# Kernel tuning notes

Measured on AMD Instinct MI355X. Metric: run time of the kernel, lower is better.

## Reference

```python
import jax, jax.numpy as jnp
import numpy as np
import math

E = 16          # num_experts
K = 2           # top_k
CAP_FACTOR = 1.25
TEMP = 1.0      # router_temperature


def setup_inputs() -> dict:
    key = jax.random.key(0)
    ks = jax.random.split(key, 4)
    B, F, H, O = 16384, 1024, 4096, 1024
    features = jax.random.normal(ks[0], (B, F), dtype=jnp.float32)
    Wg = jax.random.normal(ks[1], (E, F), dtype=jnp.float32) / np.sqrt(F)
    bg = jnp.zeros((E,), jnp.float32)
    W1 = jax.random.normal(ks[2], (E, F, H), dtype=jnp.float32) / np.sqrt(F)
    b1 = jnp.zeros((E, H), jnp.float32)
    W2 = jax.random.normal(ks[3], (E, H, O), dtype=jnp.float32) / np.sqrt(H)
    b2 = jnp.zeros((E, O), jnp.float32)
    expert_bias = jnp.zeros((E,), jnp.float32)
    return {"features": features, "Wg": Wg, "bg": bg, "W1": W1, "b1": b1,
            "W2": W2, "b2": b2, "expert_bias": expert_bias}


def reference(features, Wg, bg, W1, b1, W2, b2, expert_bias):
    B, F = features.shape
    O = W2.shape[-1]
    cap = max(1, int(math.ceil(CAP_FACTOR * B * K / E)))  # per-expert capacity

    # --- router: scores = W_g * features + expert_bias (no noise) ---
    scores = features @ Wg.T + bg + expert_bias[None, :]            # [B,E]
    topk_scores, topk_idx = jax.lax.top_k(scores, K)                # [B,K]
    topk_w = jax.nn.softmax(topk_scores / TEMP, axis=1)             # [B,K]

    # per-(token,expert) assignment and mixing weight
    onehot = topk_idx[:, :, None] == jnp.arange(E)[None, None, :]   # [B,K,E]
    assign = jnp.any(onehot, axis=1)                                # [B,E]
    w = jnp.sum(topk_w[:, :, None] * onehot.astype(topk_w.dtype), axis=1)  # [B,E]

    # capacity: first `cap` tokens (ascending index, matching torch.nonzero order)
    pos = jnp.cumsum(assign.astype(jnp.int32), axis=0) - 1          # [B,E]
    keep = assign & (pos < cap)
    pos_safe = jnp.where(keep, pos, cap)                            # dropped -> overflow slot

    # inverse map: inv[e,c] = token index filling slot c of expert e (B if empty)
    e_grid = jnp.broadcast_to(jnp.arange(E)[None, :], (B, E))
    b_grid = jnp.broadcast_to(jnp.arange(B, dtype=jnp.int32)[:, None], (B, E))
    inv = jnp.full((E, cap + 1), B, dtype=jnp.int32)
    inv = inv.at[e_grid, pos_safe].set(b_grid)[:, :cap]             # [E,cap]

    # dispatch (gather) into per-expert buffers
    feats_pad = jnp.concatenate([features, jnp.zeros((1, F), features.dtype)], axis=0)
    buf = feats_pad[inv]                                            # [E,cap,F]

    # experts: Linear -> ReLU -> Linear, batched over experts
    h = jax.nn.relu(jnp.einsum('ecf,efh->ech', buf, W1) + b1[:, None, :])
    y = jnp.einsum('ech,eho->eco', h, W2) + b2[:, None, :]          # [E,cap,O]

    # weighted combine (scatter-add back to tokens; empty slots have weight 0)
    w_pad = jnp.concatenate([w, jnp.zeros((1, E), w.dtype)], axis=0)  # [B+1,E]
    w_slot = w_pad[inv, jnp.arange(E)[:, None]]                     # [E,cap]
    out = jnp.zeros((B + 1, O), features.dtype)
    out = out.at[inv.reshape(-1)].add((w_slot[..., None] * y).reshape(-1, O))
    return out[:B]
```

## Files before the change

kernel.cpp:

```cpp
#include <hip/hip_runtime.h>
#include <math.h>


typedef __attribute__((ext_vector_type(8))) short bf16x8;
typedef __attribute__((ext_vector_type(4))) float floatx4;

static __device__ __forceinline__ unsigned short f2bf(float f) {
  union { float f; unsigned u; } v; v.f = f;
  unsigned u = v.u;
  return (unsigned short)((u + 0x7fffu + ((u >> 16) & 1u)) >> 16);
}

static __device__ __forceinline__ void gload_lds16(const void* g, void* l) {
  __builtin_amdgcn_global_load_lds(
      (const __attribute__((address_space(1))) unsigned int*)g,
      (__attribute__((address_space(3))) unsigned int*)l, 16, 0, 0);
}

__global__ void k_cvt_bf16(const float* __restrict__ src,
                           unsigned short* __restrict__ dst, long n4) {
  long i = (long)blockIdx.x * blockDim.x + threadIdx.x;
  if (i >= n4) return;
  float4 f = ((const float4*)src)[i];
  ushort4 o;
  o.x = f2bf(f.x); o.y = f2bf(f.y); o.z = f2bf(f.z); o.w = f2bf(f.w);
  ((ushort4*)dst)[i] = o;
}

__global__ void k_txp_bf16(const float* __restrict__ src,
                           unsigned short* __restrict__ dst, int Kd, int Nd) {
  __shared__ float tile[32][33];
  int e = blockIdx.z;
  int n0 = blockIdx.x * 32;
  int k0 = blockIdx.y * 32;
  int tx = threadIdx.x;
  int ty = threadIdx.y;
  const float* s = src + (size_t)e * Kd * Nd;
#pragma unroll
  for (int j = 0; j < 4; ++j) {
    int k = ty + j * 8;
    tile[k][tx] = s[(size_t)(k0 + k) * Nd + n0 + tx];
  }
  __syncthreads();
  unsigned short* d = dst + (size_t)e * Kd * Nd;
#pragma unroll
  for (int j = 0; j < 4; ++j) {
    int n = ty + j * 8;
    d[(size_t)(n0 + n) * Kd + k0 + tx] = f2bf(tile[tx][n]);
  }
}

__global__ __launch_bounds__(256) void k_gating(
    const float* __restrict__ feat, const float* __restrict__ Wg,
    const float* __restrict__ bg, const float* __restrict__ ebias,
    int* __restrict__ topki, float* __restrict__ topkw,
    int* __restrict__ hist, int B, int F) {
  __shared__ float WgS[16 * 1024];
  for (int i = threadIdx.x; i < 16 * F; i += blockDim.x) WgS[i] = Wg[i];
  __syncthreads();
  int lane = threadIdx.x & 63;
  int wid = threadIdx.x >> 6;
  int gw = blockIdx.x * 4 + wid;
  int nw = gridDim.x * 4;
  int per = B / nw;
  for (int it = 0; it < per; ++it) {
    int t = gw * per + it;
    double acc[16];
#pragma unroll
    for (int e = 0; e < 16; ++e) acc[e] = 0.0;
    const float* fr = feat + (size_t)t * F;
    for (int c = 0; c < F / 64; ++c) {
      double fd = (double)fr[c * 64 + lane];
#pragma unroll
      for (int e = 0; e < 16; ++e)
        acc[e] += fd * (double)WgS[e * F + c * 64 + lane];
    }
#pragma unroll
    for (int e = 0; e < 16; ++e) {
#pragma unroll
      for (int off = 32; off >= 1; off >>= 1)
        acc[e] += __shfl_xor(acc[e], off);
    }
    double s[16];
#pragma unroll
    for (int e = 0; e < 16; ++e)
      s[e] = acc[e] + (double)bg[e] + (double)ebias[e];
    int e1 = 0; double s1 = s[0];
#pragma unroll
    for (int e = 1; e < 16; ++e) if (s[e] > s1) { s1 = s[e]; e1 = e; }
    int e2 = -1; double s2 = -1e300;
#pragma unroll
    for (int e = 0; e < 16; ++e)
      if (e != e1 && s[e] > s2) { s2 = s[e]; e2 = e; }
    double d = exp(s2 - s1);
    float w1 = (float)(1.0 / (1.0 + d));
    float w2 = (float)(d / (1.0 + d));
    if (lane == 0) {
      topki[t * 2 + 0] = e1; topki[t * 2 + 1] = e2;
      topkw[t * 2 + 0] = w1; topkw[t * 2 + 1] = w2;
      atomicAdd(&hist[(t >> 8) * 16 + e1], 1);
      atomicAdd(&hist[(t >> 8) * 16 + e2], 1);
    }
  }
}

__global__ void k_scan(const int* __restrict__ hist, int* __restrict__ choff,
                       int* __restrict__ cntcl, int nchunk, int cap) {
  int e = threadIdx.x;
  if (e < 16) {
    int off = 0;
    for (int c = 0; c < nchunk; ++c) {
      choff[c * 16 + e] = off;
      off += hist[c * 16 + e];
    }
    cntcl[e] = off < cap ? off : cap;
  }
}

__global__ __launch_bounds__(64) void k_build(
    const int* __restrict__ topki, const float* __restrict__ topkw,
    const int* __restrict__ choff, int* __restrict__ list,
    float* __restrict__ wlist, int cap, int capR) {
  int c = blockIdx.x;
  int lane = threadIdx.x;
  int run[16];
#pragma unroll
  for (int e = 0; e < 16; ++e) run[e] = choff[c * 16 + e];
  unsigned long long below = (lane == 63) ? 0x7fffffffffffffffull
                                          : ((1ull << lane) - 1ull);
  for (int r = 0; r < 4; ++r) {
    int t = c * 256 + r * 64 + lane;
    int e1 = topki[t * 2 + 0], e2 = topki[t * 2 + 1];
    float w1 = topkw[t * 2 + 0], w2 = topkw[t * 2 + 1];
    int p1 = -1, p2 = -1;
#pragma unroll
    for (int e = 0; e < 16; ++e) {
      unsigned long long m = __ballot(e1 == e) | __ballot(e2 == e);
      int rk = run[e] + __popcll(m & below);
      if (e1 == e) p1 = rk;
      if (e2 == e) p2 = rk;
      run[e] += __popcll(m);
    }
    if (p1 >= 0 && p1 < cap) { list[e1 * capR + p1] = t; wlist[e1 * capR + p1] = w1; }
    if (p2 >= 0 && p2 < cap) { list[e2 * capR + p2] = t; wlist[e2 * capR + p2] = w2; }
  }
}

__global__ void k_padfill(const int* __restrict__ cntcl, int* __restrict__ list,
                          float* __restrict__ wlist, int capR) {
  int e = blockIdx.x;
  int cnt = cntcl[e];
  for (int s = cnt + (int)threadIdx.x; s < capR; s += (int)blockDim.x) {
    list[e * capR + s] = 0;
    wlist[e * capR + s] = 0.0f;
  }
}

#define VM_WAIT4 asm volatile("s_waitcnt vmcnt(4)" ::: "memory")
#define VM_WAIT0 asm volatile("s_waitcnt vmcnt(0)" ::: "memory")

template <int MODE>
__global__ __launch_bounds__(512, 2) void k_gemm(
    const unsigned short* __restrict__ A, const unsigned short* __restrict__ Bt,
    const float* __restrict__ bias, const int* __restrict__ list,
    const float* __restrict__ wlist, const int* __restrict__ cntcl,
    unsigned short* __restrict__ Hout, float* __restrict__ out,
    int Kd, int Nd, int RT, int NT, int capR) {
  __shared__ __align__(16) char smem[98304];

  int nwg = gridDim.x;
  int qq = nwg >> 3, rr = nwg & 7;
  int xcd = blockIdx.x & 7, idx = blockIdx.x >> 3;
  int bid = (xcd < rr ? xcd * (qq + 1) : rr * (qq + 1) + (xcd - rr) * qq) + idx;

  int e = bid / (RT * NT);
  int rt = (bid / NT) % RT;
  int nt = bid % NT;
  int cnt = cntcl[e];
  int r0 = rt * 256;
  if (r0 >= cnt) return;
  int n0 = nt * 256;

  int tid = threadIdx.x;
  int lane = tid & 63;
  int wid = tid >> 6;
  int wr = wid >> 2;
  int wc = wid & 3;
  int l16 = lane & 15, q = lane >> 4;

  int srow = wid * 16 + (lane >> 2);
  int cg = (lane & 3) ^ ((lane >> 3) & 3);
  const char* pA[2];
  const char* pB[2];
#pragma unroll
  for (int rnd = 0; rnd < 2; ++rnd) {
    int r = rnd * 128 + srow;
    const unsigned short* arow;
    if (MODE == 0) {
      int tok = list[e * capR + r0 + r];
      arow = A + (size_t)tok * Kd;
    } else {
      arow = A + (size_t)(e * capR + r0 + r) * Kd;
    }
    pA[rnd] = (const char*)arow + cg * 16;
    pB[rnd] = (const char*)(Bt + (size_t)e * Nd * Kd + (size_t)(n0 + r) * Kd) +
              cg * 16;
  }
  unsigned stbase = wid * 1024;

#define STAGE(tt, bufi)                                   \
  do {                                                    \
    char* dst_ = smem + (bufi) * 32768 + stbase;          \
    int off_ = (tt) * 64;                                 \
    gload_lds16(pA[0] + off_, dst_);                      \
    gload_lds16(pA[1] + off_, dst_ + 8192);               \
    gload_lds16(pB[0] + off_, dst_ + 16384);              \
    gload_lds16(pB[1] + off_, dst_ + 16384 + 8192);       \
  } while (0)

  floatx4 acc[8][4];
#pragma unroll
  for (int i = 0; i < 8; ++i)
#pragma unroll
    for (int j = 0; j < 4; ++j) acc[i][j] = 0.0f;

  int sw = ((q ^ ((lane >> 1) & 3)) << 4);
  int arl = wr * 128 + l16;
  int brl = wc * 64 + l16;

  int nk = Kd / 32;

  STAGE(0, 0);
  STAGE(1, 1);
  VM_WAIT4;
  __builtin_amdgcn_s_barrier();

  int cur = 0;
  for (int t = 0; t < nk; ++t) {
    const char* Ab = smem + cur * 32768;
    const char* Bb = Ab + 16384;
    bool pre = (t + 2) < nk;
    int nx2 = cur + 2; if (nx2 >= 3) nx2 -= 3;

    bf16x8 af[4], bfr[4];
#pragma unroll
    for (int i = 0; i < 4; ++i)
      af[i] = *(const bf16x8*)(Ab + (arl + i * 16) * 64 + sw);
#pragma unroll
    for (int j = 0; j < 4; ++j)
      bfr[j] = *(const bf16x8*)(Bb + (brl + j * 16) * 64 + sw);
    if (pre) STAGE(t + 2, nx2);
    __builtin_amdgcn_s_barrier();
    __builtin_amdgcn_s_setprio(1);
#pragma unroll
    for (int i = 0; i < 4; ++i)
#pragma unroll
      for (int j = 0; j < 4; ++j)
        acc[i][j] = __builtin_amdgcn_mfma_f32_16x16x32_bf16(af[i], bfr[j],
                                                            acc[i][j], 0, 0, 0);
    __builtin_amdgcn_s_setprio(0);
    __builtin_amdgcn_s_barrier();

    bf16x8 ag[4];
#pragma unroll
    for (int i = 0; i < 4; ++i)
      ag[i] = *(const bf16x8*)(Ab + (arl + 64 + i * 16) * 64 + sw);
    __builtin_amdgcn_s_barrier();
    __builtin_amdgcn_s_setprio(1);
#pragma unroll
    for (int i = 0; i < 4; ++i)
#pragma unroll
      for (int j = 0; j < 4; ++j)
        acc[4 + i][j] = __builtin_amdgcn_mfma_f32_16x16x32_bf16(
            ag[i], bfr[j], acc[4 + i][j], 0, 0, 0);
    __builtin_amdgcn_s_setprio(0);
    if (pre) { VM_WAIT4; } else { VM_WAIT0; }
    __builtin_amdgcn_s_barrier();
    cur = (cur + 1 == 3) ? 0 : cur + 1;
  }
#undef STAGE

  float bv[4];
#pragma unroll
  for (int j = 0; j < 4; ++j)
    bv[j] = bias[(size_t)e * Nd + n0 + wc * 64 + j * 16 + l16];

  if (MODE == 0) {
#pragma unroll
    for (int i = 0; i < 8; ++i) {
      int rowb = r0 + wr * 128 + i * 16 + q * 4;
#pragma unroll
      for (int j = 0; j < 4; ++j) {
        int col = n0 + wc * 64 + j * 16 + l16;
#pragma unroll
        for (int r = 0; r < 4; ++r) {
          float v = acc[i][j][r] + bv[j];
          v = v > 0.0f ? v : 0.0f;
          Hout[(size_t)(e * capR + rowb + r) * Nd + col] = f2bf(v);
        }
      }
    }
  } else {
#pragma unroll
    for (int i = 0; i < 8; ++i) {
      int rowb = r0 + wr * 128 + i * 16 + q * 4;
      int tok[4]; float wv[4];
#pragma unroll
      for (int r = 0; r < 4; ++r) {
        tok[r] = list[e * capR + rowb + r];
        wv[r] = wlist[e * capR + rowb + r];
      }
#pragma unroll
      for (int j = 0; j < 4; ++j) {
        int col = n0 + wc * 64 + j * 16 + l16;
#pragma unroll
        for (int r = 0; r < 4; ++r) {
          float v = (acc[i][j][r] + bv[j]) * wv[r];
          atomicAdd(&out[(size_t)tok[r] * Nd + col], v);
        }
      }
    }
  }
}

extern "C" void kernel_launch(void* const* d_in, const int* in_sizes, int n_in,
                              void* d_out, int out_size, void* d_ws,
                              size_t ws_size, hipStream_t stream) {
  const float* feat  = (const float*)d_in[0];
  const float* Wg    = (const float*)d_in[1];
  const float* bg    = (const float*)d_in[2];
  const float* W1    = (const float*)d_in[3];
  const float* b1    = (const float*)d_in[4];
  const float* W2    = (const float*)d_in[5];
  const float* b2    = (const float*)d_in[6];
  const float* ebias = (const float*)d_in[7];

  const int E = 16;
  const int B = 16384, F = 1024, Hd = 4096, O = 1024;
  const int cap = 2560;
  const int capR = 2560;
  const int nchunk = B / 256;
  const int RT = capR / 256;

  char* p = (char*)d_ws;
  auto carve = [&](size_t bytes) {
    char* r = p;
    p += (bytes + 255) & ~(size_t)255;
    return r;
  };
  unsigned short* featbf = (unsigned short*)carve((size_t)B * F * 2);
  unsigned short* W1T = (unsigned short*)carve((size_t)E * Hd * F * 2);
  unsigned short* W2T = (unsigned short*)carve((size_t)E * O * Hd * 2);
  unsigned short* Hbuf = (unsigned short*)carve((size_t)E * capR * Hd * 2);
  int* topki = (int*)carve((size_t)B * 2 * 4);
  float* topkw = (float*)carve((size_t)B * 2 * 4);
  int* hist = (int*)carve((size_t)nchunk * 16 * 4);
  int* choff = (int*)carve((size_t)nchunk * 16 * 4);
  int* cntcl = (int*)carve(16 * 4);
  int* list = (int*)carve((size_t)E * capR * 4);
  float* wlist = (float*)carve((size_t)E * capR * 4);

  hipMemsetAsync(d_out, 0, (size_t)B * O * sizeof(float), stream);
  hipMemsetAsync(hist, 0, (size_t)nchunk * 16 * 4, stream);

  k_cvt_bf16<<<(B * F / 4 + 255) / 256, 256, 0, stream>>>(feat, featbf,
                                                          (long)B * F / 4);
  dim3 tb(32, 8);
  k_txp_bf16<<<dim3(Hd / 32, F / 32, E), tb, 0, stream>>>(W1, W1T, F, Hd);
  k_txp_bf16<<<dim3(O / 32, Hd / 32, E), tb, 0, stream>>>(W2, W2T, Hd, O);
  k_gating<<<256, 256, 0, stream>>>(feat, Wg, bg, ebias, topki, topkw, hist, B, F);
  k_scan<<<1, 64, 0, stream>>>(hist, choff, cntcl, nchunk, cap);
  k_build<<<nchunk, 64, 0, stream>>>(topki, topkw, choff, list, wlist, cap, capR);
  k_padfill<<<E, 256, 0, stream>>>(cntcl, list, wlist, capR);

  k_gemm<0><<<E * RT * (Hd / 256), 512, 0, stream>>>(
      featbf, W1T, b1, list, wlist, cntcl, Hbuf, nullptr, F, Hd, RT, Hd / 256,
      capR);
  k_gemm<1><<<E * RT * (O / 256), 512, 0, stream>>>(
      Hbuf, W2T, b2, list, wlist, cntcl, nullptr, (float*)d_out, Hd, O, RT,
      O / 256, capR);
}
```

Measured before the change: 1.760 ms.

## Shrink GEMM tiles to 128x128 and replace atomic scatter with gather combine

The expert GEMMs now use 128x128 tiles with 256 threads, double-buffered LDS (32 KB) and a simpler one-stage prefetch pipeline, allowing three workgroups per CU. The second GEMM no longer does weighted atomicAdd into the output. It writes per-slot fp32 results to a buffer that aliases the bf16 feature buffer, and a new combine kernel gathers each token's two slots and writes the output directly, which also drops the output memset. The intent is to remove atomic contention and improve occupancy. The cost is lower per-tile data reuse, a weaker prefetch depth, and an extra 160 MB intermediate write and read.

```diff
diff --git a/kernel.cpp b/kernel.cpp
--- a/kernel.cpp
+++ b/kernel.cpp
@@ -118,9 +118,8 @@
 }
 
 __global__ __launch_bounds__(64) void k_build(
-    const int* __restrict__ topki, const float* __restrict__ topkw,
-    const int* __restrict__ choff, int* __restrict__ list,
-    float* __restrict__ wlist, int cap, int capR) {
+    const int* __restrict__ topki, const int* __restrict__ choff,
+    int* __restrict__ list, int* __restrict__ slots, int cap, int capR) {
   int c = blockIdx.x;
   int lane = threadIdx.x;
   int run[16];
@@ -131,7 +130,6 @@
   for (int r = 0; r < 4; ++r) {
     int t = c * 256 + r * 64 + lane;
     int e1 = topki[t * 2 + 0], e2 = topki[t * 2 + 1];
-    float w1 = topkw[t * 2 + 0], w2 = topkw[t * 2 + 1];
     int p1 = -1, p2 = -1;
 #pragma unroll
     for (int e = 0; e < 16; ++e) {
@@ -141,32 +139,30 @@
       if (e2 == e) p2 = rk;
       run[e] += __popcll(m);
     }
-    if (p1 >= 0 && p1 < cap) { list[e1 * capR + p1] = t; wlist[e1 * capR + p1] = w1; }
-    if (p2 >= 0 && p2 < cap) { list[e2 * capR + p2] = t; wlist[e2 * capR + p2] = w2; }
+    if (p1 < cap) list[e1 * capR + p1] = t;
+    if (p2 < cap) list[e2 * capR + p2] = t;
+    slots[t * 2 + 0] = (p1 < cap) ? p1 : -1;
+    slots[t * 2 + 1] = (p2 < cap) ? p2 : -1;
   }
 }
 
 __global__ void k_padfill(const int* __restrict__ cntcl, int* __restrict__ list,
-                          float* __restrict__ wlist, int capR) {
+                          int capR) {
   int e = blockIdx.x;
   int cnt = cntcl[e];
-  for (int s = cnt + (int)threadIdx.x; s < capR; s += (int)blockDim.x) {
+  for (int s = cnt + (int)threadIdx.x; s < capR; s += (int)blockDim.x)
     list[e * capR + s] = 0;
-    wlist[e * capR + s] = 0.0f;
-  }
-}
-
-#define VM_WAIT4 asm volatile("s_waitcnt vmcnt(4)" ::: "memory")
+}
+
 #define VM_WAIT0 asm volatile("s_waitcnt vmcnt(0)" ::: "memory")
 
 template <int MODE>
-__global__ __launch_bounds__(512, 2) void k_gemm(
+__global__ __launch_bounds__(256, 3) void k_gemm(
     const unsigned short* __restrict__ A, const unsigned short* __restrict__ Bt,
     const float* __restrict__ bias, const int* __restrict__ list,
-    const float* __restrict__ wlist, const int* __restrict__ cntcl,
-    unsigned short* __restrict__ Hout, float* __restrict__ out,
-    int Kd, int Nd, int RT, int NT, int capR) {
-  __shared__ __align__(16) char smem[98304];
+    const int* __restrict__ cntcl, unsigned short* __restrict__ Hout,
+    float* __restrict__ Yout, int Kd, int Nd, int RT, int NT, int capR) {
+  __shared__ __align__(16) char smem[32768];
 
   int nwg = gridDim.x;
   int qq = nwg >> 3, rr = nwg & 7;
@@ -177,71 +173,67 @@
   int rt = (bid / NT) % RT;
   int nt = bid % NT;
   int cnt = cntcl[e];
-  int r0 = rt * 256;
+  int r0 = rt * 128;
   if (r0 >= cnt) return;
-  int n0 = nt * 256;
+  int n0 = nt * 128;
 
   int tid = threadIdx.x;
   int lane = tid & 63;
   int wid = tid >> 6;
-  int wr = wid >> 2;
-  int wc = wid & 3;
+  int wr = wid >> 1;
+  int wc = wid & 1;
   int l16 = lane & 15, q = lane >> 4;
 
-  int srow = wid * 16 + (lane >> 2);
-  int cg = (lane & 3) ^ ((lane >> 3) & 3);
-  const char* pA[2];
-  const char* pB[2];
-#pragma unroll
-  for (int rnd = 0; rnd < 2; ++rnd) {
-    int r = rnd * 128 + srow;
-    const unsigned short* arow;
-    if (MODE == 0) {
-      int tok = list[e * capR + r0 + r];
-      arow = A + (size_t)tok * Kd;
-    } else {
-      arow = A + (size_t)(e * capR + r0 + r) * Kd;
-    }
-    pA[rnd] = (const char*)arow + cg * 16;
-    pB[rnd] = (const char*)(Bt + (size_t)e * Nd * Kd + (size_t)(n0 + r) * Kd) +
-              cg * 16;
-  }
+  int srow = tid >> 2;
+  int cg = (tid & 3) ^ ((srow >> 1) & 3);
+  const char* pA0;
+  const char* pA1;
+  if (MODE == 0) {
+    int tok0 = list[e * capR + r0 + srow];
+    int tok1 = list[e * capR + r0 + srow + 64];
+    pA0 = (const char*)(A + (size_t)tok0 * Kd) + cg * 16;
+    pA1 = (const char*)(A + (size_t)tok1 * Kd) + cg * 16;
+  } else {
+    pA0 = (const char*)(A + (size_t)(e * capR + r0 + srow) * Kd) + cg * 16;
+    pA1 = pA0 + (size_t)64 * Kd * 2;
+  }
+  const char* pB0 =
+      (const char*)(Bt + (size_t)e * Nd * Kd + (size_t)(n0 + srow) * Kd) +
+      cg * 16;
+  const char* pB1 = pB0 + (size_t)64 * Kd * 2;
   unsigned stbase = wid * 1024;
 
-#define STAGE(tt, bufi)                                   \
-  do {                                                    \
-    char* dst_ = smem + (bufi) * 32768 + stbase;          \
-    int off_ = (tt) * 64;                                 \
-    gload_lds16(pA[0] + off_, dst_);                      \
-    gload_lds16(pA[1] + off_, dst_ + 8192);               \
-    gload_lds16(pB[0] + off_, dst_ + 16384);              \
-    gload_lds16(pB[1] + off_, dst_ + 16384 + 8192);       \
+#define STAGE(tt, bufi)                                  \
+  do {                                                   \
+    char* dst_ = smem + (bufi) * 16384 + stbase;         \
+    int off_ = (tt) * 64;                                \
+    gload_lds16(pA0 + off_, dst_);                       \
+    gload_lds16(pA1 + off_, dst_ + 4096);                \
+    gload_lds16(pB0 + off_, dst_ + 8192);                \
+    gload_lds16(pB1 + off_, dst_ + 12288);               \
   } while (0)
 
-  floatx4 acc[8][4];
-#pragma unroll
-  for (int i = 0; i < 8; ++i)
+  floatx4 acc[4][4];
+#pragma unroll
+  for (int i = 0; i < 4; ++i)
 #pragma unroll
     for (int j = 0; j < 4; ++j) acc[i][j] = 0.0f;
 
-  int sw = ((q ^ ((lane >> 1) & 3)) << 4);
-  int arl = wr * 128 + l16;
+  int sw = ((q ^ ((l16 >> 1) & 3)) << 4);
+  int arl = wr * 64 + l16;
   int brl = wc * 64 + l16;
 
   int nk = Kd / 32;
 
   STAGE(0, 0);
-  STAGE(1, 1);
-  VM_WAIT4;
+  VM_WAIT0;
   __builtin_amdgcn_s_barrier();
 
   int cur = 0;
   for (int t = 0; t < nk; ++t) {
-    const char* Ab = smem + cur * 32768;
-    const char* Bb = Ab + 16384;
-    bool pre = (t + 2) < nk;
-    int nx2 = cur + 2; if (nx2 >= 3) nx2 -= 3;
-
+    const char* Ab = smem + cur * 16384;
+    const char* Bb = Ab + 8192;
+    if (t + 1 < nk) STAGE(t + 1, cur ^ 1);
     bf16x8 af[4], bfr[4];
 #pragma unroll
     for (int i = 0; i < 4; ++i)
@@ -249,8 +241,6 @@
 #pragma unroll
     for (int j = 0; j < 4; ++j)
       bfr[j] = *(const bf16x8*)(Bb + (brl + j * 16) * 64 + sw);
-    if (pre) STAGE(t + 2, nx2);
-    __builtin_amdgcn_s_barrier();
     __builtin_amdgcn_s_setprio(1);
 #pragma unroll
     for (int i = 0; i < 4; ++i)
@@ -259,24 +249,9 @@
         acc[i][j] = __builtin_amdgcn_mfma_f32_16x16x32_bf16(af[i], bfr[j],
                                                             acc[i][j], 0, 0, 0);
     __builtin_amdgcn_s_setprio(0);
+    VM_WAIT0;
     __builtin_amdgcn_s_barrier();
-
-    bf16x8 ag[4];
-#pragma unroll
-    for (int i = 0; i < 4; ++i)
-      ag[i] = *(const bf16x8*)(Ab + (arl + 64 + i * 16) * 64 + sw);
-    __builtin_amdgcn_s_barrier();
-    __builtin_amdgcn_s_setprio(1);
-#pragma unroll
-    for (int i = 0; i < 4; ++i)
-#pragma unroll
-      for (int j = 0; j < 4; ++j)
-        acc[4 + i][j] = __builtin_amdgcn_mfma_f32_16x16x32_bf16(
-            ag[i], bfr[j], acc[4 + i][j], 0, 0, 0);
-    __builtin_amdgcn_s_setprio(0);
-    if (pre) { VM_WAIT4; } else { VM_WAIT0; }
-    __builtin_amdgcn_s_barrier();
-    cur = (cur + 1 == 3) ? 0 : cur + 1;
+    cur ^= 1;
   }
 #undef STAGE
 
@@ -287,8 +262,8 @@
 
   if (MODE == 0) {
 #pragma unroll
-    for (int i = 0; i < 8; ++i) {
-      int rowb = r0 + wr * 128 + i * 16 + q * 4;
+    for (int i = 0; i < 4; ++i) {
+      int rowb = r0 + wr * 64 + i * 16 + q * 4;
 #pragma unroll
       for (int j = 0; j < 4; ++j) {
         int col = n0 + wc * 64 + j * 16 + l16;
@@ -302,25 +277,38 @@
     }
   } else {
 #pragma unroll
-    for (int i = 0; i < 8; ++i) {
-      int rowb = r0 + wr * 128 + i * 16 + q * 4;
-      int tok[4]; float wv[4];
-#pragma unroll
-      for (int r = 0; r < 4; ++r) {
-        tok[r] = list[e * capR + rowb + r];
-        wv[r] = wlist[e * capR + rowb + r];
-      }
+    for (int i = 0; i < 4; ++i) {
+      int rowb = r0 + wr * 64 + i * 16 + q * 4;
 #pragma unroll
       for (int j = 0; j < 4; ++j) {
         int col = n0 + wc * 64 + j * 16 + l16;
 #pragma unroll
-        for (int r = 0; r < 4; ++r) {
-          float v = (acc[i][j][r] + bv[j]) * wv[r];
-          atomicAdd(&out[(size_t)tok[r] * Nd + col], v);
-        }
+        for (int r = 0; r < 4; ++r)
+          Yout[(size_t)(e * capR + rowb + r) * Nd + col] = acc[i][j][r] + bv[j];
       }
     }
   }
+}
+
+__global__ __launch_bounds__(256) void k_combine(
+    const float* __restrict__ Y, const int* __restrict__ topki,
+    const float* __restrict__ topkw, const int* __restrict__ slots,
+    float* __restrict__ out, int capR, int O) {
+  int t = blockIdx.x;
+  int c = threadIdx.x;
+  int e1 = topki[t * 2 + 0], e2 = topki[t * 2 + 1];
+  int s1 = slots[t * 2 + 0], s2 = slots[t * 2 + 1];
+  float w1 = topkw[t * 2 + 0], w2 = topkw[t * 2 + 1];
+  float4 r = make_float4(0.f, 0.f, 0.f, 0.f);
+  if (s1 >= 0) {
+    float4 a = ((const float4*)(Y + (size_t)(e1 * capR + s1) * O))[c];
+    r.x += w1 * a.x; r.y += w1 * a.y; r.z += w1 * a.z; r.w += w1 * a.w;
+  }
+  if (s2 >= 0) {
+    float4 b = ((const float4*)(Y + (size_t)(e2 * capR + s2) * O))[c];
+    r.x += w2 * b.x; r.y += w2 * b.y; r.z += w2 * b.z; r.w += w2 * b.w;
+  }
+  ((float4*)(out + (size_t)t * O))[c] = r;
 }
 
 extern "C" void kernel_launch(void* const* d_in, const int* in_sizes, int n_in,
@@ -340,7 +328,7 @@
   const int cap = 2560;
   const int capR = 2560;
   const int nchunk = B / 256;
-  const int RT = capR / 256;
+  const int RT = capR / 128;
 
   char* p = (char*)d_ws;
   auto carve = [&](size_t bytes) {
@@ -358,9 +346,9 @@
   int* choff = (int*)carve((size_t)nchunk * 16 * 4);
   int* cntcl = (int*)carve(16 * 4);
   int* list = (int*)carve((size_t)E * capR * 4);
-  float* wlist = (float*)carve((size_t)E * capR * 4);
-
-  hipMemsetAsync(d_out, 0, (size_t)B * O * sizeof(float), stream);
+  int* slots = (int*)carve((size_t)B * 2 * 4);
+  float* Ybuf = (float*)featbf;
+
   hipMemsetAsync(hist, 0, (size_t)nchunk * 16 * 4, stream);
 
   k_cvt_bf16<<<(B * F / 4 + 255) / 256, 256, 0, stream>>>(feat, featbf,
@@ -370,13 +358,13 @@
   k_txp_bf16<<<dim3(O / 32, Hd / 32, E), tb, 0, stream>>>(W2, W2T, Hd, O);
   k_gating<<<256, 256, 0, stream>>>(feat, Wg, bg, ebias, topki, topkw, hist, B, F);
   k_scan<<<1, 64, 0, stream>>>(hist, choff, cntcl, nchunk, cap);
-  k_build<<<nchunk, 64, 0, stream>>>(topki, topkw, choff, list, wlist, cap, capR);
-  k_padfill<<<E, 256, 0, stream>>>(cntcl, list, wlist, capR);
-
-  k_gemm<0><<<E * RT * (Hd / 256), 512, 0, stream>>>(
-      featbf, W1T, b1, list, wlist, cntcl, Hbuf, nullptr, F, Hd, RT, Hd / 256,
-      capR);
-  k_gemm<1><<<E * RT * (O / 256), 512, 0, stream>>>(
-      Hbuf, W2T, b2, list, wlist, cntcl, nullptr, (float*)d_out, Hd, O, RT,
-      O / 256, capR);
-}
+  k_build<<<nchunk, 64, 0, stream>>>(topki, choff, list, slots, cap, capR);
+  k_padfill<<<E, 256, 0, stream>>>(cntcl, list, capR);
+
+  k_gemm<0><<<E * RT * (Hd / 128), 256, 0, stream>>>(
+      featbf, W1T, b1, list, cntcl, Hbuf, nullptr, F, Hd, RT, Hd / 128, capR);
+  k_gemm<1><<<E * RT * (O / 128), 256, 0, stream>>>(
+      Hbuf, W2T, b2, list, cntcl, nullptr, Ybuf, Hd, O, RT, O / 128, capR);
+  k_combine<<<B, 256, 0, stream>>>(Ybuf, topki, topkw, slots, (float*)d_out,
+                                   capR, O);
+}
```

After: 1.537 ms. 12.6% less time.
